# Kernel optimization log

Measured on AMD Instinct MI355X. Metric: run time of the kernel, lower is better.

Reference implementation:

```python
import jax, jax.numpy as jnp
import numpy as np

D_MODEL, D_SLOT, D_HIDDEN = 256, 256, 128


def setup_inputs() -> dict:
    key = jax.random.key(0)
    k1, k2, k3, k4, k5, k6 = jax.random.split(key, 6)
    B, T, N = 8, 1024, 64
    features = jax.random.normal(k1, (B, T, D_MODEL), dtype=jnp.float32)
    slots = jax.random.normal(k2, (B, N, D_SLOT), dtype=jnp.float32)
    # nn.Linear-style init (uniform +- 1/sqrt(fan_in))
    lim1 = 1.0 / np.sqrt(D_MODEL + D_SLOT)
    W_proj = jax.random.uniform(k3, (D_MODEL + D_SLOT, D_HIDDEN), minval=-lim1, maxval=lim1, dtype=jnp.float32)
    b_proj = jax.random.uniform(k4, (D_HIDDEN,), minval=-lim1, maxval=lim1, dtype=jnp.float32)
    lim2 = 1.0 / np.sqrt(D_HIDDEN)
    w_head = jax.random.uniform(k5, (D_HIDDEN,), minval=-lim2, maxval=lim2, dtype=jnp.float32)
    b_head = jax.random.uniform(k6, (), minval=-lim2, maxval=lim2, dtype=jnp.float32)
    return {"features": features, "slots": slots, "W_proj": W_proj, "b_proj": b_proj, "w_head": w_head, "b_head": b_head}


def reference(features, slots, W_proj, b_proj, w_head, b_head):
    # proj(concat([feat, slot])) is separable: feat @ W_f + slot @ W_s + b
    W_f = W_proj[:D_MODEL]   # (D, H)
    W_s = W_proj[D_MODEL:]   # (S, H)
    f_proj = jnp.einsum('btd,dh->bth', features, W_f)          # (B, T, H)
    s_proj = jnp.einsum('bns,sh->bnh', slots, W_s) + b_proj    # (B, N, H)
    x = jax.nn.relu(f_proj[:, :, None, :] + s_proj[:, None, :, :])  # (B, T, N, H)
    out = jnp.einsum('btnh,h->btn', x, w_head) + b_head         # (B, T, N)
    return out
```

## Files before the change

kernel.cpp:

```cpp
#include <hip/hip_runtime.h>
#include <hip/hip_bf16.h>

typedef unsigned short ushort_t;
typedef __attribute__((ext_vector_type(8))) short short8;
typedef __attribute__((ext_vector_type(4))) float f32x4;

__device__ __forceinline__ ushort_t f2bf(float f) {
    unsigned v;
    __builtin_memcpy(&v, &f, 4);
    unsigned r = (v + 0x7FFFu + ((v >> 16) & 1u)) >> 16;
    return (ushort_t)r;
}

__global__ __launch_bounds__(128) void asd_k1(
        const float* __restrict__ slots,
        const float* __restrict__ Wproj,
        const float* __restrict__ bproj,
        float* __restrict__ sT,
        ushort_t* __restrict__ Wpack) {
    int bid = blockIdx.x;
    int tid = threadIdx.x;
    if (bid < 512) {
        __shared__ float sl[256];
        int b = bid >> 6, n = bid & 63;
        const float* srow = slots + (b * 64 + n) * 256;
        float2 v = ((const float2*)srow)[tid];
        sl[2 * tid]     = v.x;
        sl[2 * tid + 1] = v.y;
        __syncthreads();
        int h = tid;
        float acc = bproj[h];
        const float* Wcol = Wproj + 256 * 128 + h;
        #pragma unroll 8
        for (int d = 0; d < 256; ++d) {
            acc += sl[d] * Wcol[d * 128];
        }
        sT[(b * 128 + h) * 64 + n] = acc;
    } else {
        int gid = (bid - 512) * 128 + tid;
        int l   = gid & 63;
        int idx = gid >> 6;
        int kb  = idx >> 3, nt = idx & 7;
        int r0  = kb * 32 + ((l >> 4) << 3);
        int c   = nt * 16 + (l & 15);
        short8 frag;
        #pragma unroll
        for (int i = 0; i < 8; ++i)
            frag[i] = (short)f2bf(Wproj[(r0 + i) * 128 + c]);
        ((short8*)Wpack)[gid] = frag;
    }
}

__global__ __launch_bounds__(256) void asd_k2(
        const float* __restrict__ feat,
        const float* __restrict__ sT,
        const ushort_t* __restrict__ Wpack,
        const float* __restrict__ whead,
        const float* __restrict__ bhead,
        float* __restrict__ out) {
    __shared__ float lds_s[128 * 68];
    __shared__ float lds_f[16 * 132];
    __shared__ float lds_w[128];

    int tid = threadIdx.x;
    int bid = blockIdx.x;
    int b   = bid >> 6;
    int t0  = (bid & 63) << 4;

    const f32x4* src   = (const f32x4*)(sT + b * 128 * 64);
    f32x4*       ldsS4 = (f32x4*)lds_s;
    #pragma unroll
    for (int r = 0; r < 8; ++r) {
        int i4 = r * 256 + tid;
        int h  = i4 >> 4, c4 = i4 & 15;
        ldsS4[h * 17 + c4] = src[i4];
    }
    if (tid < 128) lds_w[tid] = whead[tid];
    float bh = bhead[0];

    int l = tid & 63;
    int w = tid >> 6;
    int m = l & 15, q = l >> 4;
    int nt0 = 2 * w;
    f32x4 acc0 = {0.f, 0.f, 0.f, 0.f};
    f32x4 acc1 = {0.f, 0.f, 0.f, 0.f};
    const short8* Wp = (const short8*)Wpack;
    #pragma unroll
    for (int kb = 0; kb < 8; ++kb) {
        const float* arow = feat + (b * 1024 + t0 + m) * 256 + kb * 32 + q * 8;
        f32x4 af0 = *(const f32x4*)arow;
        f32x4 af1 = *(const f32x4*)(arow + 4);
        short8 A;
        #pragma unroll
        for (int i = 0; i < 4; ++i) {
            A[i]     = (short)f2bf(af0[i]);
            A[4 + i] = (short)f2bf(af1[i]);
        }
        short8 B0 = Wp[(kb * 8 + nt0) * 64 + l];
        short8 B1 = Wp[(kb * 8 + nt0 + 1) * 64 + l];
        acc0 = __builtin_amdgcn_mfma_f32_16x16x32_bf16(A, B0, acc0, 0, 0, 0);
        acc1 = __builtin_amdgcn_mfma_f32_16x16x32_bf16(A, B1, acc1, 0, 0, 0);
    }
    #pragma unroll
    for (int r = 0; r < 4; ++r) {
        int row = q * 4 + r;
        lds_f[row * 132 + nt0 * 16 + m]       = acc0[r];
        lds_f[row * 132 + (nt0 + 1) * 16 + m] = acc1[r];
    }
    __syncthreads();

    int t = tid >> 4, ng = tid & 15;
    const f32x4* fR = (const f32x4*)(lds_f + t * 132);
    float a0 = bh, a1 = bh, a2 = bh, a3 = bh;
    #pragma unroll 8
    for (int h4 = 0; h4 < 32; ++h4) {
        f32x4 f4 = fR[h4];
        #pragma unroll
        for (int i = 0; i < 4; ++i) {
            int h = h4 * 4 + i;
            f32x4 s4 = ldsS4[h * 17 + ng];
            float wv = lds_w[h];
            float x0 = fmaxf(f4[i] + s4[0], 0.f);
            float x1 = fmaxf(f4[i] + s4[1], 0.f);
            float x2 = fmaxf(f4[i] + s4[2], 0.f);
            float x3 = fmaxf(f4[i] + s4[3], 0.f);
            a0 += x0 * wv;
            a1 += x1 * wv;
            a2 += x2 * wv;
            a3 += x3 * wv;
        }
    }
    f32x4 o = {a0, a1, a2, a3};
    *(f32x4*)(out + (b * 1024 + t0 + t) * 64 + 4 * ng) = o;
}

extern "C" void kernel_launch(void* const* d_in, const int* in_sizes, int n_in,
                              void* d_out, int out_size, void* d_ws, size_t ws_size,
                              hipStream_t stream) {
    const float* feat  = (const float*)d_in[0];
    const float* slots = (const float*)d_in[1];
    const float* Wproj = (const float*)d_in[2];
    const float* bproj = (const float*)d_in[3];
    const float* whead = (const float*)d_in[4];
    const float* bhead = (const float*)d_in[5];
    float* out = (float*)d_out;

    float*    sT    = (float*)d_ws;
    ushort_t* Wpack = (ushort_t*)((char*)d_ws + 262144);

    hipLaunchKernelGGL(asd_k1, dim3(544), dim3(128), 0, stream,
                       slots, Wproj, bproj, sT, Wpack);
    hipLaunchKernelGGL(asd_k2, dim3(512), dim3(256), 0, stream,
                       feat, sT, Wpack, whead, bhead, out);
}
```

Baseline: 92.80 us.

## Use packed fp16 with fdot2 for relu-head reduction and split slot projection

Slot projections and feature projections are stored as fp16 pairs, and the head reduction uses packed half2 add, max and fdot2 with fp32 accumulation instead of scalar fp32 math. This halves LDS traffic and instruction count in the dominant T×N×H loop. The slot-projection kernel also splits the reduction dimension across two halves of a 512-thread block and handles two slots per block. Rounding to fp16 before the relu lowers accuracy of the summed output.

New measurement: 82.09 us. -11.5%, faster.

```diff
diff --git a/kernel.cpp b/kernel.cpp
--- a/kernel.cpp
+++ b/kernel.cpp
@@ -1,9 +1,19 @@
 #include <hip/hip_runtime.h>
 #include <hip/hip_bf16.h>
+#include <hip/hip_fp16.h>
 
 typedef unsigned short ushort_t;
+typedef unsigned int uint_t;
 typedef __attribute__((ext_vector_type(8))) short short8;
 typedef __attribute__((ext_vector_type(4))) float f32x4;
+typedef __attribute__((ext_vector_type(4))) unsigned int uint4v;
+typedef __attribute__((ext_vector_type(2))) _Float16 half2v;
+
+#if defined(__has_builtin)
+#if __has_builtin(__builtin_amdgcn_fdot2)
+#define HAVE_FDOT2 1
+#endif
+#endif
 
 __device__ __forceinline__ ushort_t f2bf(float f) {
     unsigned v;
@@ -12,32 +22,43 @@
     return (ushort_t)r;
 }
 
-__global__ __launch_bounds__(128) void asd_k1(
+__global__ __launch_bounds__(512) void asd_k1(
         const float* __restrict__ slots,
         const float* __restrict__ Wproj,
         const float* __restrict__ bproj,
-        float* __restrict__ sT,
+        ushort_t* __restrict__ s2,
         ushort_t* __restrict__ Wpack) {
     int bid = blockIdx.x;
     int tid = threadIdx.x;
-    if (bid < 512) {
-        __shared__ float sl[256];
-        int b = bid >> 6, n = bid & 63;
-        const float* srow = slots + (b * 64 + n) * 256;
-        float2 v = ((const float2*)srow)[tid];
-        sl[2 * tid]     = v.x;
-        sl[2 * tid + 1] = v.y;
+    if (bid < 256) {
+        __shared__ float sl[512];
+        __shared__ float part[256];
+        int b  = bid >> 5;
+        int n0 = (bid & 31) * 2;
+        sl[tid] = slots[(b * 64 + n0) * 256 + tid];
         __syncthreads();
-        int h = tid;
-        float acc = bproj[h];
-        const float* Wcol = Wproj + 256 * 128 + h;
+        int dh = tid >> 8;
+        int hn = tid & 255;
+        int nl = hn >> 7;
+        int h  = hn & 127;
+        const float* Wcol = Wproj + 256 * 128 + dh * 128 * 128 + h;
+        const float* srow = sl + nl * 256 + dh * 128;
+        float acc = 0.f;
         #pragma unroll 8
-        for (int d = 0; d < 256; ++d) {
-            acc += sl[d] * Wcol[d * 128];
+        for (int d = 0; d < 128; ++d)
+            acc += srow[d] * Wcol[d * 128];
+        if (dh) part[hn] = acc;
+        __syncthreads();
+        if (!dh) {
+            float v = acc + part[hn] + bproj[h];
+            _Float16 hv = (_Float16)v;
+            ushort_t u;
+            __builtin_memcpy(&u, &hv, 2);
+            int n = n0 + nl;
+            s2[b * 8192 + (h >> 1) * 128 + n * 2 + (h & 1)] = u;
         }
-        sT[(b * 128 + h) * 64 + n] = acc;
     } else {
-        int gid = (bid - 512) * 128 + tid;
+        int gid = (bid - 256) * 512 + tid;
         int l   = gid & 63;
         int idx = gid >> 6;
         int kb  = idx >> 3, nt = idx & 7;
@@ -53,29 +74,33 @@
 
 __global__ __launch_bounds__(256) void asd_k2(
         const float* __restrict__ feat,
-        const float* __restrict__ sT,
+        const ushort_t* __restrict__ s2g,
         const ushort_t* __restrict__ Wpack,
         const float* __restrict__ whead,
         const float* __restrict__ bhead,
         float* __restrict__ out) {
-    __shared__ float lds_s[128 * 68];
-    __shared__ float lds_f[16 * 132];
-    __shared__ float lds_w[128];
+    __shared__ uint_t   s2_lds[64 * 68];
+    __shared__ ushort_t f_lds[16 * 132];
+    __shared__ uint_t   w2_lds[64];
 
     int tid = threadIdx.x;
     int bid = blockIdx.x;
     int b   = bid >> 6;
     int t0  = (bid & 63) << 4;
 
-    const f32x4* src   = (const f32x4*)(sT + b * 128 * 64);
-    f32x4*       ldsS4 = (f32x4*)lds_s;
+    const uint4v* src = (const uint4v*)(s2g + b * 8192);
     #pragma unroll
-    for (int r = 0; r < 8; ++r) {
+    for (int r = 0; r < 4; ++r) {
         int i4 = r * 256 + tid;
-        int h  = i4 >> 4, c4 = i4 & 15;
-        ldsS4[h * 17 + c4] = src[i4];
+        int h2 = i4 >> 4, c = i4 & 15;
+        *(uint4v*)(s2_lds + h2 * 68 + c * 4) = src[i4];
     }
-    if (tid < 128) lds_w[tid] = whead[tid];
+    if (tid < 64) {
+        half2v w2 = { (_Float16)whead[2 * tid], (_Float16)whead[2 * tid + 1] };
+        uint_t u;
+        __builtin_memcpy(&u, &w2, 4);
+        w2_lds[tid] = u;
+    }
     float bh = bhead[0];
 
     int l = tid & 63;
@@ -104,30 +129,42 @@
     #pragma unroll
     for (int r = 0; r < 4; ++r) {
         int row = q * 4 + r;
-        lds_f[row * 132 + nt0 * 16 + m]       = acc0[r];
-        lds_f[row * 132 + (nt0 + 1) * 16 + m] = acc1[r];
+        _Float16 v0 = (_Float16)acc0[r];
+        _Float16 v1 = (_Float16)acc1[r];
+        ushort_t u0, u1;
+        __builtin_memcpy(&u0, &v0, 2);
+        __builtin_memcpy(&u1, &v1, 2);
+        f_lds[row * 132 + nt0 * 16 + m]       = u0;
+        f_lds[row * 132 + (nt0 + 1) * 16 + m] = u1;
     }
     __syncthreads();
 
     int t = tid >> 4, ng = tid & 15;
-    const f32x4* fR = (const f32x4*)(lds_f + t * 132);
+    const ushort_t* fR = f_lds + t * 132;
     float a0 = bh, a1 = bh, a2 = bh, a3 = bh;
+    const half2v hz = { (_Float16)0.f, (_Float16)0.f };
     #pragma unroll 8
-    for (int h4 = 0; h4 < 32; ++h4) {
-        f32x4 f4 = fR[h4];
+    for (int h2 = 0; h2 < 64; ++h2) {
+        uint_t fu = *(const uint_t*)(fR + 2 * h2);
+        half2v f2;
+        __builtin_memcpy(&f2, &fu, 4);
+        uint4v s4 = *(const uint4v*)(s2_lds + h2 * 68 + 4 * ng);
+        uint_t wu = w2_lds[h2];
+        half2v w2;
+        __builtin_memcpy(&w2, &wu, 4);
+        float* accs[4] = {&a0, &a1, &a2, &a3};
         #pragma unroll
-        for (int i = 0; i < 4; ++i) {
-            int h = h4 * 4 + i;
-            f32x4 s4 = ldsS4[h * 17 + ng];
-            float wv = lds_w[h];
-            float x0 = fmaxf(f4[i] + s4[0], 0.f);
-            float x1 = fmaxf(f4[i] + s4[1], 0.f);
-            float x2 = fmaxf(f4[i] + s4[2], 0.f);
-            float x3 = fmaxf(f4[i] + s4[3], 0.f);
-            a0 += x0 * wv;
-            a1 += x1 * wv;
-            a2 += x2 * wv;
-            a3 += x3 * wv;
+        for (int j = 0; j < 4; ++j) {
+            uint_t su = s4[j];
+            half2v sv;
+            __builtin_memcpy(&sv, &su, 4);
+            half2v x = f2 + sv;
+            x = __builtin_elementwise_max(x, hz);
+#ifdef HAVE_FDOT2
+            *accs[j] = __builtin_amdgcn_fdot2(x, w2, *accs[j], false);
+#else
+            *accs[j] += (float)x[0] * (float)w2[0] + (float)x[1] * (float)w2[1];
+#endif
         }
     }
     f32x4 o = {a0, a1, a2, a3};
@@ -145,11 +182,11 @@
     const float* bhead = (const float*)d_in[5];
     float* out = (float*)d_out;
 
-    float*    sT    = (float*)d_ws;
-    ushort_t* Wpack = (ushort_t*)((char*)d_ws + 262144);
+    ushort_t* s2    = (ushort_t*)d_ws;
+    ushort_t* Wpack = (ushort_t*)((char*)d_ws + 131072);
 
-    hipLaunchKernelGGL(asd_k1, dim3(544), dim3(128), 0, stream,
-                       slots, Wproj, bproj, sT, Wpack);
+    hipLaunchKernelGGL(asd_k1, dim3(264), dim3(512), 0, stream,
+                       slots, Wproj, bproj, s2, Wpack);
     hipLaunchKernelGGL(asd_k2, dim3(512), dim3(256), 0, stream,
-                       feat, sT, Wpack, whead, bhead, out);
+                       feat, s2, Wpack, whead, bhead, out);
 }
```
